# Kernel tuning notes

Hardware: AMD Instinct MI355X
Metric: run time of the kernel (lower is better)

## Reference

```python
import jax, jax.numpy as jnp
import numpy as np

# Circuit hyperparameters (match init_kwargs)
N_QUBITS = 10
N_LAYERS = 5          # hardware_efficient_ansatz layers (data re-uploading)
N_ACTIONS = 2         # CartPole-v1 discrete action space
BETA = 1.0
DIM = 2 ** N_QUBITS

# Bit table: wire 0 is the most-significant bit (PennyLane convention).
_bits = ((np.arange(DIM)[:, None] >> (N_QUBITS - 1 - np.arange(N_QUBITS))) & 1)

# Diagonal of the ring of CZ gates: product over pairs (i, i+1 mod n) of (-1)^{b_i b_j}.
_s = np.ones(DIM)
for _i in range(N_QUBITS):
    _j = (_i + 1) % N_QUBITS
    _s *= 1.0 - 2.0 * (_bits[:, _i] * _bits[:, _j])
CZ_DIAG = jnp.asarray(_s, dtype=jnp.complex64)

# Z^{\otimes n} observable diagonal: (-1)^{popcount(k)}
Z_SIGN = jnp.asarray(1.0 - 2.0 * (_bits.sum(1) % 2), dtype=jnp.float32)


def _rx(t):
    c = jnp.cos(0.5 * t).astype(jnp.complex64)
    s = jnp.sin(0.5 * t).astype(jnp.complex64)
    return jnp.stack([jnp.stack([c, -1j * s], -1), jnp.stack([-1j * s, c], -1)], -2)


def _ry(t):
    c = jnp.cos(0.5 * t).astype(jnp.complex64)
    s = jnp.sin(0.5 * t).astype(jnp.complex64)
    return jnp.stack([jnp.stack([c, -s], -1), jnp.stack([s, c], -1)], -2)


def _rz(t):
    e = jnp.exp(-0.5j * t.astype(jnp.complex64))
    z = jnp.zeros_like(e)
    return jnp.stack([jnp.stack([e, z], -1), jnp.stack([z, jnp.conj(e)], -1)], -2)


def _apply_1q(state, U, q):
    """Apply a single-qubit gate on wire q. state: [B, 2^n]; U: [2,2] or [B,2,2]."""
    B = state.shape[0]
    s = state.reshape(B, 2 ** q, 2, -1)
    if U.ndim == 2:
        s = jnp.einsum('ij,bljr->blir', U, s)
    else:
        s = jnp.einsum('bij,bljr->blir', U, s)
    return s.reshape(B, DIM)


def _variational_layer(state, t):
    """Per-qubit Rx,Ry,Rz rotations (t: [n_qubits,3]) followed by a CZ ring."""
    for q in range(N_QUBITS):
        U = _rz(t[q, 2]) @ _ry(t[q, 1]) @ _rx(t[q, 0])  # RX applied first
        state = _apply_1q(state, U, q)
    return state * CZ_DIAG


def setup_inputs() -> dict:
    key = jax.random.key(0)
    k1, k2 = jax.random.split(key)
    x = jax.random.normal(k1, (2048, N_QUBITS), jnp.float32)
    # _theta = rand(total_theta) * pi ; total_theta = (L+1)*n*3
    theta = jax.random.uniform(k2, ((N_LAYERS + 1) * N_QUBITS * 3,), jnp.float32) * np.pi
    # _lambda = ones(total_inputs) ; total_inputs = L*n
    lam = jnp.ones((N_LAYERS * N_QUBITS,), jnp.float32)
    # Alternating(n_actions): weight row initialized to alternating signs
    w = jnp.asarray([[(-1.0) ** i for i in range(N_ACTIONS)]], jnp.float32)
    return {"x": x, "theta": theta, "lam": lam, "w": w}


def reference(x, theta, lam, w):
    B = x.shape[0]
    th = theta.reshape(N_LAYERS + 1, N_QUBITS, 3)
    lm = lam.reshape(N_LAYERS, N_QUBITS)  # scaled_inputs = x_tiled * lambda
    state = jnp.zeros((B, DIM), jnp.complex64).at[:, 0].set(1.0)
    for l in range(N_LAYERS):
        state = _variational_layer(state, th[l])
        ang = x * lm[l]                      # [B, n] encoding angles for this layer
        for q in range(N_QUBITS):
            state = _apply_1q(state, _rx(ang[:, q]), q)
    state = _variational_layer(state, th[N_LAYERS])
    # <Z x Z x ... x Z>
    exp_z = jnp.sum((state.real ** 2 + state.imag ** 2) * Z_SIGN, axis=1)  # [B]
    logits = exp_z[:, None] * w * BETA       # [B,1] @ [1,n_actions], scaled by beta
    return jax.nn.softmax(logits, axis=1)
```

## Files before the change

kernel.cpp:

```cpp
#include <hip/hip_runtime.h>

#define NQ 10
#define NL 5

typedef float v2f __attribute__((ext_vector_type(2)));

__device__ __forceinline__ v2f sp(float s) { v2f r = { s, s }; return r; }

template <int M>
__device__ __forceinline__ float lane_xor(float v, int lane) {
    unsigned u = __float_as_uint(v);
    if constexpr (M == 1) {
        return __uint_as_float((unsigned)__builtin_amdgcn_update_dpp(0, (int)u, 0xB1, 0xF, 0xF, true));
    } else if constexpr (M == 2) {
        return __uint_as_float((unsigned)__builtin_amdgcn_update_dpp(0, (int)u, 0x4E, 0xF, 0xF, true));
    } else if constexpr (M == 4) {
        return __uint_as_float((unsigned)__builtin_amdgcn_ds_swizzle((int)u, 0x101F));
    } else if constexpr (M == 8) {
        return __uint_as_float((unsigned)__builtin_amdgcn_update_dpp(0, (int)u, 0x128, 0xF, 0xF, true));
    } else if constexpr (M == 16) {
#if __has_builtin(__builtin_amdgcn_permlane16_swap)
        auto r = __builtin_amdgcn_permlane16_swap(u, u, false, false);
        return __uint_as_float((lane & 16) ? r[0] : r[1]);
#else
        return __uint_as_float((unsigned)__builtin_amdgcn_ds_swizzle((int)u, 0x401F));
#endif
    } else {
#if __has_builtin(__builtin_amdgcn_permlane32_swap)
        auto r = __builtin_amdgcn_permlane32_swap(u, u, false, false);
        return __uint_as_float((lane & 32) ? r[0] : r[1]);
#else
        return __shfl_xor(v, 32, 64);
#endif
    }
}

__device__ __forceinline__ void make_u(float tx, float ty, float tz,
                                       float& u00r, float& u00i, float& u01r, float& u01i,
                                       float& u10r, float& u10i, float& u11r, float& u11i) {
    float cx, sx, cy, sy, cz, sz;
    __sincosf(0.5f * tx, &sx, &cx);
    __sincosf(0.5f * ty, &sy, &cy);
    __sincosf(0.5f * tz, &sz, &cz);
    u00r =  cz * cy * cx + sz * sy * sx;
    u00i =  cz * sy * sx - sz * cy * cx;
    u01r = -cz * sy * cx - sz * cy * sx;
    u01i =  sz * sy * cx - cz * cy * sx;
    u10r = -u01r;  u10i =  u01i;
    u11r =  u00r;  u11i = -u00i;
}

__global__ void pqc_setup(const float* __restrict__ theta, float* __restrict__ gm) {
    int g = threadIdx.x;
    if (g >= (NL + 1) * NQ) return;
    const float* th = theta + g * 3;
    float u00r, u00i, u01r, u01i, u10r, u10i, u11r, u11i;
    make_u(th[0], th[1], th[2], u00r, u00i, u01r, u01i, u10r, u10i, u11r, u11i);
    float* o = gm + g * 16;
    o[0] = u00r;  o[1] = u00i;  o[2] = u01r;  o[3] = u01i;
    o[4] = u10r;  o[5] = u10i;  o[6] = u11r;  o[7] = u11i;
    o[8]  = u01i; o[9]  = -u01r; o[10] = u00i; o[11] = -u00r;
    o[12] = u11i; o[13] = -u11r; o[14] = u10i; o[15] = -u10r;
}

template <int P>
__device__ __forceinline__ void apply_p(v2f fr[8], v2f fi[8], const float wv[8], int lane) {
    const float w00r = wv[0], w00i = wv[1], w01r = wv[2], w01i = wv[3];
    const float w10r = wv[4], w10i = wv[5], w11r = wv[6], w11i = wv[7];
    if constexpr (P == 0) {
        v2f c0r = { w00r, w11r }, c0i = { w00i, w11i };
        v2f c1r = { w01r, w10r }, c1i = { w01i, w10i };
#pragma unroll
        for (int j = 0; j < 8; ++j) {
            v2f ar = fr[j], ai = fi[j];
            v2f srp = ar.yx, sip = ai.yx;
            fr[j] = c0r * ar - c0i * ai + c1r * srp - c1i * sip;
            fi[j] = c0r * ai + c0i * ar + c1r * sip + c1i * srp;
        }
    } else if constexpr (P < 4) {
        constexpr int LJ = 1 << (P - 1);
        v2f a00r = sp(w00r), a00i = sp(w00i), a01r = sp(w01r), a01i = sp(w01i);
        v2f a10r = sp(w10r), a10i = sp(w10i), a11r = sp(w11r), a11i = sp(w11i);
#pragma unroll
        for (int base = 0; base < 8; ++base) {
            if (base & LJ) continue;
            v2f a0r = fr[base], a0i = fi[base];
            v2f a1r = fr[base | LJ], a1i = fi[base | LJ];
            fr[base]      = a00r * a0r - a00i * a0i + a01r * a1r - a01i * a1i;
            fi[base]      = a00r * a0i + a00i * a0r + a01r * a1i + a01i * a1r;
            fr[base | LJ] = a10r * a0r - a10i * a0i + a11r * a1r - a11i * a1i;
            fi[base | LJ] = a10r * a0i + a10i * a0r + a11r * a1i + a11i * a1r;
        }
    } else {
        constexpr int M = 1 << (P - 4);
        const int bit = (lane >> (P - 4)) & 1;
        v2f pr = sp(bit ? w11r : w00r), pi = sp(bit ? w11i : w00i);
        v2f qr = sp(bit ? w10r : w01r), qi = sp(bit ? w10i : w01i);
#pragma unroll
        for (int j = 0; j < 8; ++j) {
            v2f ofr, ofi;
            ofr.x = lane_xor<M>(fr[j].x, lane);
            ofr.y = lane_xor<M>(fr[j].y, lane);
            ofi.x = lane_xor<M>(fi[j].x, lane);
            ofi.y = lane_xor<M>(fi[j].y, lane);
            v2f nr = pr * fr[j] - pi * fi[j] + qr * ofr - qi * ofi;
            v2f ni = pr * fi[j] + pi * fr[j] + qr * ofi + qi * ofr;
            fr[j] = nr;
            fi[j] = ni;
        }
    }
}

__device__ __forceinline__ void apply_layer(v2f fr[8], v2f fi[8], const float W[NQ][8],
                                            const v2f sv[8], int lane) {
    apply_p<9>(fr, fi, W[0], lane);
    apply_p<8>(fr, fi, W[1], lane);
    apply_p<7>(fr, fi, W[2], lane);
    apply_p<6>(fr, fi, W[3], lane);
    apply_p<5>(fr, fi, W[4], lane);
    apply_p<4>(fr, fi, W[5], lane);
    apply_p<3>(fr, fi, W[6], lane);
    apply_p<2>(fr, fi, W[7], lane);
    apply_p<1>(fr, fi, W[8], lane);
    apply_p<0>(fr, fi, W[9], lane);
#pragma unroll
    for (int j = 0; j < 8; ++j) { fr[j] *= sv[j]; fi[j] *= sv[j]; }
}

__global__ void __launch_bounds__(64, 2) pqc_kernel(const float* __restrict__ x,
                                                    const float* __restrict__ lam,
                                                    const float* __restrict__ w,
                                                    const float* __restrict__ gm,
                                                    float* __restrict__ out, int B) {
    const int lane = threadIdx.x;
    const int b = blockIdx.x;

    v2f fr[8], fi[8];
#pragma unroll
    for (int j = 0; j < 8; ++j) { fr[j] = sp(0.f); fi[j] = sp(0.f); }
    if (lane == 0) fr[0].x = 1.f;

    v2f sv[8];
    unsigned zmask = 0;
#pragma unroll
    for (int j = 0; j < 8; ++j) {
#pragma unroll
        for (int h = 0; h < 2; ++h) {
            int k = (lane << 4) | (2 * j + h);
            int par = (__popc(k & (k >> 1)) + ((k & (k >> 9)) & 1)) & 1;
            float s = __uint_as_float(0x3f800000u | ((unsigned)par << 31));
            if (h == 0) sv[j].x = s; else sv[j].y = s;
            zmask |= (unsigned)(__popc(k) & 1) << (2 * j + h);
        }
    }

    float xr[NQ];
#pragma unroll
    for (int q = 0; q < NQ; ++q) xr[q] = x[b * NQ + q];

    {
        float W[NQ][8];
#pragma unroll
        for (int q = 0; q < NQ; ++q)
#pragma unroll
            for (int t = 0; t < 8; ++t) W[q][t] = gm[q * 16 + t];
        apply_layer(fr, fi, W, sv, lane);
    }

#pragma unroll
    for (int l = 1; l <= NL; ++l) {
        const float* lm = lam + (l - 1) * NQ;
        float cc[NQ], ss[NQ];
#pragma unroll
        for (int q = 0; q < NQ; ++q)
            __sincosf(0.5f * xr[q] * lm[q], &ss[q], &cc[q]);
        float W[NQ][8];
#pragma unroll
        for (int q = 0; q < NQ; ++q) {
            const float* g = gm + (l * NQ + q) * 16;
#pragma unroll
            for (int t = 0; t < 8; ++t) W[q][t] = cc[q] * g[t] + ss[q] * g[8 + t];
        }
        apply_layer(fr, fi, W, sv, lane);
    }

    v2f acc = sp(0.f);
#pragma unroll
    for (int j = 0; j < 8; ++j) {
        v2f zs;
        zs.x = __uint_as_float(0x3f800000u | (((zmask >> (2 * j)) & 1u) << 31));
        zs.y = __uint_as_float(0x3f800000u | (((zmask >> (2 * j + 1)) & 1u) << 31));
        acc += zs * (fr[j] * fr[j] + fi[j] * fi[j]);
    }
    float ez = acc.x + acc.y;
    ez += lane_xor<1>(ez, lane);
    ez += lane_xor<2>(ez, lane);
    ez += lane_xor<4>(ez, lane);
    ez += lane_xor<8>(ez, lane);
    ez += lane_xor<16>(ez, lane);
    ez += lane_xor<32>(ez, lane);

    if (lane == 0) {
        float l0 = ez * w[0], l1 = ez * w[1];
        float m = fmaxf(l0, l1);
        float e0 = __expf(l0 - m), e1 = __expf(l1 - m);
        float inv = 1.f / (e0 + e1);
        out[2 * b + 0] = e0 * inv;
        out[2 * b + 1] = e1 * inv;
    }
}

extern "C" void kernel_launch(void* const* d_in, const int* in_sizes, int n_in,
                              void* d_out, int out_size, void* d_ws, size_t ws_size,
                              hipStream_t stream) {
    const float* x     = (const float*)d_in[0];
    const float* theta = (const float*)d_in[1];
    const float* lam   = (const float*)d_in[2];
    const float* w     = (const float*)d_in[3];
    float* out = (float*)d_out;
    float* gm  = (float*)d_ws;

    const int B = in_sizes[0] / NQ;
    hipLaunchKernelGGL(pqc_setup, dim3(1), dim3(64), 0, stream, theta, gm);
    hipLaunchKernelGGL(pqc_kernel, dim3(B), dim3(64), 0, stream,
                       x, lam, w, gm, out, B);
}
```

Baseline: 90.26 us.

## Process two batch samples per wavefront and use both permlane swap outputs

Each 64-lane block now simulates two circuits (two batch elements) in interleaved register sets, halving the grid, so independent instruction streams can hide cross-lane permute and sincos latency. For wires mapped to lane-distance 16 and 32, both halves returned by permlane swap are used directly with lane-selected coefficients, which removes the per-element select. The layer loop is folded into one rolled loop, with the first layer using a zero encoding angle so it shares the same code. This doubles register pressure under launch_bounds(64,2) and assumes B is even and that the permlane swap builtins exist.

```diff
diff --git a/kernel.cpp b/kernel.cpp
--- a/kernel.cpp
+++ b/kernel.cpp
@@ -8,7 +8,7 @@
 __device__ __forceinline__ v2f sp(float s) { v2f r = { s, s }; return r; }
 
 template <int M>
-__device__ __forceinline__ float lane_xor(float v, int lane) {
+__device__ __forceinline__ float lane_xor_direct(float v) {
     unsigned u = __float_as_uint(v);
     if constexpr (M == 1) {
         return __uint_as_float((unsigned)__builtin_amdgcn_update_dpp(0, (int)u, 0xB1, 0xF, 0xF, true));
@@ -16,22 +16,31 @@
         return __uint_as_float((unsigned)__builtin_amdgcn_update_dpp(0, (int)u, 0x4E, 0xF, 0xF, true));
     } else if constexpr (M == 4) {
         return __uint_as_float((unsigned)__builtin_amdgcn_ds_swizzle((int)u, 0x101F));
-    } else if constexpr (M == 8) {
+    } else {
         return __uint_as_float((unsigned)__builtin_amdgcn_update_dpp(0, (int)u, 0x128, 0xF, 0xF, true));
-    } else if constexpr (M == 16) {
-#if __has_builtin(__builtin_amdgcn_permlane16_swap)
+    }
+}
+
+template <int M>
+__device__ __forceinline__ void lane_swap_pair(float v, float& r0, float& r1) {
+    unsigned u = __float_as_uint(v);
+    if constexpr (M == 16) {
         auto r = __builtin_amdgcn_permlane16_swap(u, u, false, false);
-        return __uint_as_float((lane & 16) ? r[0] : r[1]);
-#else
-        return __uint_as_float((unsigned)__builtin_amdgcn_ds_swizzle((int)u, 0x401F));
-#endif
-    } else {
-#if __has_builtin(__builtin_amdgcn_permlane32_swap)
+        r0 = __uint_as_float(r[0]); r1 = __uint_as_float(r[1]);
+    } else {
         auto r = __builtin_amdgcn_permlane32_swap(u, u, false, false);
-        return __uint_as_float((lane & 32) ? r[0] : r[1]);
-#else
-        return __shfl_xor(v, 32, 64);
-#endif
+        r0 = __uint_as_float(r[0]); r1 = __uint_as_float(r[1]);
+    }
+}
+
+template <int M>
+__device__ __forceinline__ float lane_xor(float v, int lane) {
+    if constexpr (M < 16) {
+        return lane_xor_direct<M>(v);
+    } else {
+        float r0, r1;
+        lane_swap_pair<M>(v, r0, r1);
+        return (lane & M) ? r0 : r1;
     }
 }
 
@@ -91,7 +100,7 @@
             fr[base | LJ] = a10r * a0r - a10i * a0i + a11r * a1r - a11i * a1i;
             fi[base | LJ] = a10r * a0i + a10i * a0r + a11r * a1i + a11i * a1r;
         }
-    } else {
+    } else if constexpr (P < 8) {
         constexpr int M = 1 << (P - 4);
         const int bit = (lane >> (P - 4)) & 1;
         v2f pr = sp(bit ? w11r : w00r), pi = sp(bit ? w11i : w00i);
@@ -99,33 +108,47 @@
 #pragma unroll
         for (int j = 0; j < 8; ++j) {
             v2f ofr, ofi;
-            ofr.x = lane_xor<M>(fr[j].x, lane);
-            ofr.y = lane_xor<M>(fr[j].y, lane);
-            ofi.x = lane_xor<M>(fi[j].x, lane);
-            ofi.y = lane_xor<M>(fi[j].y, lane);
+            ofr.x = lane_xor_direct<M>(fr[j].x);
+            ofr.y = lane_xor_direct<M>(fr[j].y);
+            ofi.x = lane_xor_direct<M>(fi[j].x);
+            ofi.y = lane_xor_direct<M>(fi[j].y);
             v2f nr = pr * fr[j] - pi * fi[j] + qr * ofr - qi * ofi;
             v2f ni = pr * fi[j] + pi * fr[j] + qr * ofi + qi * ofr;
             fr[j] = nr;
             fi[j] = ni;
         }
-    }
-}
-
-__device__ __forceinline__ void apply_layer(v2f fr[8], v2f fi[8], const float W[NQ][8],
-                                            const v2f sv[8], int lane) {
-    apply_p<9>(fr, fi, W[0], lane);
-    apply_p<8>(fr, fi, W[1], lane);
-    apply_p<7>(fr, fi, W[2], lane);
-    apply_p<6>(fr, fi, W[3], lane);
-    apply_p<5>(fr, fi, W[4], lane);
-    apply_p<4>(fr, fi, W[5], lane);
-    apply_p<3>(fr, fi, W[6], lane);
-    apply_p<2>(fr, fi, W[7], lane);
-    apply_p<1>(fr, fi, W[8], lane);
-    apply_p<0>(fr, fi, W[9], lane);
-#pragma unroll
-    for (int j = 0; j < 8; ++j) { fr[j] *= sv[j]; fi[j] *= sv[j]; }
-}
+    } else {
+        constexpr int M = 1 << (P - 4);
+        const bool hi = (lane & M) != 0;
+        v2f cAr = sp(hi ? w10r : w00r), cAi = sp(hi ? w10i : w00i);
+        v2f cBr = sp(hi ? w11r : w01r), cBi = sp(hi ? w11i : w01i);
+#pragma unroll
+        for (int j = 0; j < 8; ++j) {
+            float a0x, a1x, a0y, a1y, b0x, b1x, b0y, b1y;
+            lane_swap_pair<M>(fr[j].x, a0x, a1x);
+            lane_swap_pair<M>(fr[j].y, a0y, a1y);
+            lane_swap_pair<M>(fi[j].x, b0x, b1x);
+            lane_swap_pair<M>(fi[j].y, b0y, b1y);
+            v2f A0r = { a0x, a0y }, A1r = { a1x, a1y };
+            v2f A0i = { b0x, b0y }, A1i = { b1x, b1y };
+            fr[j] = cAr * A0r - cAi * A0i + cBr * A1r - cBi * A1i;
+            fi[j] = cAr * A0i + cAi * A0r + cBr * A1i + cBi * A1r;
+        }
+    }
+}
+
+#define GATE2(qq, PP)                                                              \
+    {                                                                              \
+        const float* g = gl + (qq) * 16;                                           \
+        float W0[8], W1[8];                                                        \
+        _Pragma("unroll")                                                          \
+        for (int t = 0; t < 8; ++t) {                                              \
+            W0[t] = cc0[qq] * g[t] + ss0[qq] * g[8 + t];                           \
+            W1[t] = cc1[qq] * g[t] + ss1[qq] * g[8 + t];                           \
+        }                                                                          \
+        apply_p<PP>(fr0, fi0, W0, lane);                                           \
+        apply_p<PP>(fr1, fi1, W1, lane);                                           \
+    }
 
 __global__ void __launch_bounds__(64, 2) pqc_kernel(const float* __restrict__ x,
                                                     const float* __restrict__ lam,
@@ -133,12 +156,16 @@
                                                     const float* __restrict__ gm,
                                                     float* __restrict__ out, int B) {
     const int lane = threadIdx.x;
-    const int b = blockIdx.x;
-
-    v2f fr[8], fi[8];
-#pragma unroll
-    for (int j = 0; j < 8; ++j) { fr[j] = sp(0.f); fi[j] = sp(0.f); }
-    if (lane == 0) fr[0].x = 1.f;
+    const int b0 = blockIdx.x * 2;
+    const int b1 = b0 + 1;
+
+    v2f fr0[8], fi0[8], fr1[8], fi1[8];
+#pragma unroll
+    for (int j = 0; j < 8; ++j) {
+        fr0[j] = sp(0.f); fi0[j] = sp(0.f);
+        fr1[j] = sp(0.f); fi1[j] = sp(0.f);
+    }
+    if (lane == 0) { fr0[0].x = 1.f; fr1[0].x = 1.f; }
 
     v2f sv[8];
     unsigned zmask = 0;
@@ -154,59 +181,68 @@
         }
     }
 
-    float xr[NQ];
-#pragma unroll
-    for (int q = 0; q < NQ; ++q) xr[q] = x[b * NQ + q];
-
-    {
-        float W[NQ][8];
-#pragma unroll
-        for (int q = 0; q < NQ; ++q)
-#pragma unroll
-            for (int t = 0; t < 8; ++t) W[q][t] = gm[q * 16 + t];
-        apply_layer(fr, fi, W, sv, lane);
-    }
-
-#pragma unroll
-    for (int l = 1; l <= NL; ++l) {
-        const float* lm = lam + (l - 1) * NQ;
-        float cc[NQ], ss[NQ];
-#pragma unroll
-        for (int q = 0; q < NQ; ++q)
-            __sincosf(0.5f * xr[q] * lm[q], &ss[q], &cc[q]);
-        float W[NQ][8];
+    float xr0[NQ], xr1[NQ];
+#pragma unroll
+    for (int q = 0; q < NQ; ++q) {
+        xr0[q] = x[b0 * NQ + q];
+        xr1[q] = x[b1 * NQ + q];
+    }
+
+    for (int l = 0; l <= NL; ++l) {
+        const float* gl = gm + l * NQ * 16;
+        const float* lm = lam + (l > 0 ? (l - 1) * NQ : 0);
+        const float en = (l > 0) ? 0.5f : 0.0f;
+        float cc0[NQ], ss0[NQ], cc1[NQ], ss1[NQ];
 #pragma unroll
         for (int q = 0; q < NQ; ++q) {
-            const float* g = gm + (l * NQ + q) * 16;
-#pragma unroll
-            for (int t = 0; t < 8; ++t) W[q][t] = cc[q] * g[t] + ss[q] * g[8 + t];
-        }
-        apply_layer(fr, fi, W, sv, lane);
-    }
-
-    v2f acc = sp(0.f);
+            __sincosf(en * xr0[q] * lm[q], &ss0[q], &cc0[q]);
+            __sincosf(en * xr1[q] * lm[q], &ss1[q], &cc1[q]);
+        }
+        GATE2(0, 9) GATE2(1, 8) GATE2(2, 7) GATE2(3, 6) GATE2(4, 5)
+        GATE2(5, 4) GATE2(6, 3) GATE2(7, 2) GATE2(8, 1) GATE2(9, 0)
+#pragma unroll
+        for (int j = 0; j < 8; ++j) {
+            fr0[j] *= sv[j]; fi0[j] *= sv[j];
+            fr1[j] *= sv[j]; fi1[j] *= sv[j];
+        }
+    }
+
+    v2f acc0 = sp(0.f), acc1 = sp(0.f);
 #pragma unroll
     for (int j = 0; j < 8; ++j) {
         v2f zs;
         zs.x = __uint_as_float(0x3f800000u | (((zmask >> (2 * j)) & 1u) << 31));
         zs.y = __uint_as_float(0x3f800000u | (((zmask >> (2 * j + 1)) & 1u) << 31));
-        acc += zs * (fr[j] * fr[j] + fi[j] * fi[j]);
-    }
-    float ez = acc.x + acc.y;
-    ez += lane_xor<1>(ez, lane);
-    ez += lane_xor<2>(ez, lane);
-    ez += lane_xor<4>(ez, lane);
-    ez += lane_xor<8>(ez, lane);
-    ez += lane_xor<16>(ez, lane);
-    ez += lane_xor<32>(ez, lane);
+        acc0 += zs * (fr0[j] * fr0[j] + fi0[j] * fi0[j]);
+        acc1 += zs * (fr1[j] * fr1[j] + fi1[j] * fi1[j]);
+    }
+    float ez0 = acc0.x + acc0.y;
+    float ez1 = acc1.x + acc1.y;
+    ez0 += lane_xor<1>(ez0, lane);   ez1 += lane_xor<1>(ez1, lane);
+    ez0 += lane_xor<2>(ez0, lane);   ez1 += lane_xor<2>(ez1, lane);
+    ez0 += lane_xor<4>(ez0, lane);   ez1 += lane_xor<4>(ez1, lane);
+    ez0 += lane_xor<8>(ez0, lane);   ez1 += lane_xor<8>(ez1, lane);
+    ez0 += lane_xor<16>(ez0, lane);  ez1 += lane_xor<16>(ez1, lane);
+    ez0 += lane_xor<32>(ez0, lane);  ez1 += lane_xor<32>(ez1, lane);
 
     if (lane == 0) {
-        float l0 = ez * w[0], l1 = ez * w[1];
-        float m = fmaxf(l0, l1);
-        float e0 = __expf(l0 - m), e1 = __expf(l1 - m);
-        float inv = 1.f / (e0 + e1);
-        out[2 * b + 0] = e0 * inv;
-        out[2 * b + 1] = e1 * inv;
+        float w0 = w[0], w1 = w[1];
+        {
+            float l0 = ez0 * w0, l1 = ez0 * w1;
+            float m = fmaxf(l0, l1);
+            float e0 = __expf(l0 - m), e1 = __expf(l1 - m);
+            float inv = 1.f / (e0 + e1);
+            out[2 * b0 + 0] = e0 * inv;
+            out[2 * b0 + 1] = e1 * inv;
+        }
+        {
+            float l0 = ez1 * w0, l1 = ez1 * w1;
+            float m = fmaxf(l0, l1);
+            float e0 = __expf(l0 - m), e1 = __expf(l1 - m);
+            float inv = 1.f / (e0 + e1);
+            out[2 * b1 + 0] = e0 * inv;
+            out[2 * b1 + 1] = e1 * inv;
+        }
     }
 }
 
@@ -222,6 +258,6 @@
 
     const int B = in_sizes[0] / NQ;
     hipLaunchKernelGGL(pqc_setup, dim3(1), dim3(64), 0, stream, theta, gm);
-    hipLaunchKernelGGL(pqc_kernel, dim3(B), dim3(64), 0, stream,
+    hipLaunchKernelGGL(pqc_kernel, dim3(B / 2), dim3(64), 0, stream,
                        x, lam, w, gm, out, B);
 }
```

Result: slower. 101.2 us (+12.1%).
